# Kernel tuning notes

Measured on AMD Instinct MI355X. Metric: run time of the kernel, lower is better.

## Reference

```python
import jax, jax.numpy as jnp
import numpy as np

N_MODES = 256
N_LAYERS = 4


def _fourier_layer(inp, x, fw_l, lw_l):
    # inp: [B, n_modes] layer state; x: [B, 3] coords
    # tf.signal.rfftnd(..., fft_length=[n_modes]) crops/pads the last axis to
    # n_modes, i.e. uses the first n_modes entries of concat([x, inp], -1).
    d = jnp.concatenate([x, inp], axis=-1)[:, :N_MODES]        # [B, n_modes]
    F = jnp.fft.rfft(d, n=N_MODES, axis=-1)                    # [B, n_modes//2+1]
    x_spatial = jnp.fft.irfft(F * fw_l.astype(F.dtype), n=N_MODES, axis=-1)
    x_spatial = x_spatial.astype(jnp.float32)
    z = inp[:, :N_MODES] * lw_l                                # linear residual branch
    return jax.nn.relu(x_spatial + z)


def setup_inputs() -> dict:
    key = jax.random.key(0)
    ks = jax.random.split(key, 6)
    B, P1, P2, P3 = 262144, 64, N_MODES, 1
    mu = jax.random.normal(ks[0], (B, P1), dtype=jnp.float32)
    x = jax.random.normal(ks[1], (B, 3), dtype=jnp.float32)
    W1 = jax.random.normal(ks[2], (P1, P2), dtype=jnp.float32) * (2.0 / P1) ** 0.5
    b1 = jnp.zeros((P2,), dtype=jnp.float32)
    fw = jax.random.normal(ks[3], (N_LAYERS, N_MODES // 2 + 1), dtype=jnp.float32)
    lw = jax.random.normal(ks[4], (N_LAYERS, N_MODES), dtype=jnp.float32) * 0.1
    W2 = jax.random.normal(ks[5], (P2, P3), dtype=jnp.float32) * (1.0 / P2) ** 0.5
    b2 = jnp.zeros((P3,), dtype=jnp.float32)
    return {"mu": mu, "x": x, "W1": W1, "b1": b1, "fw": fw, "lw": lw, "W2": W2, "b2": b2}


def reference(mu, x, W1, b1, fw, lw, W2, b2):
    # encoder (first_network): dense + relu  -> [B, p_2]
    h = jax.nn.relu(mu @ W1 + b1)
    # stack of Fourier layers (small, structurally distinct loop over n_layers)
    for l in range(N_LAYERS):
        h = _fourier_layer(h, x, fw[l], lw[l])
    # decoder (last_network): dense -> [B, p_3]
    return h @ W2 + b2
```

## Files before the change

### kernel.cpp

```cpp
#include <hip/hip_runtime.h>

#define N_B   262144
#define BM    128
#define KAUG  288
#define LDA   264
#define LHX   32

typedef _Float16 f16x8 __attribute__((ext_vector_type(8)));
typedef _Float16 f16x4 __attribute__((ext_vector_type(4)));
typedef float    f32x4 __attribute__((ext_vector_type(4)));

__global__ void fno_precompute(const float* __restrict__ W1,
                               const float* __restrict__ fw,
                               const float* __restrict__ lw,
                               _Float16* __restrict__ Mt,
                               _Float16* __restrict__ W1t)
{
    const int t = threadIdx.x;
    const int b = blockIdx.x;
    if (b < 64) {
        const int l  = b >> 4;
        const int ng = b & 15;
        __shared__ float cosTab[256];
        __shared__ float cs[256];
        cosTab[t] = cosf((float)t * (6.28318530717958647692f / 256.0f));
        __syncthreads();
        {
            const float* fwl = fw + l * 129;
            float s = fwl[0];
            #pragma unroll 4
            for (int k = 1; k < 128; ++k)
                s += 2.0f * fwl[k] * cosTab[(k * t) & 255];
            s += fwl[128] * ((t & 1) ? -1.0f : 1.0f);
            cs[t] = s * (1.0f / 256.0f);
        }
        __syncthreads();
        for (int idx = t; idx < 16 * KAUG; idx += 256) {
            const int n = ng * 16 + idx / KAUG;
            const int k = idx % KAUG;
            float v = 0.0f;
            if (k < 253)               v = cs[(n - k - 3) & 255];
            if (k == n)                v += lw[l * 256 + n];
            if (k >= 256 && k < 259)   v = cs[(n - (k - 256)) & 255];
            Mt[((size_t)l * 256 + n) * KAUG + k] = (_Float16)v;
        }
    } else {
        const int base = (b - 64) * 4096;
        #pragma unroll
        for (int i = 0; i < 16; ++i) {
            const int idx = base + t + i * 256;
            const int n = idx >> 6, k = idx & 63;
            W1t[idx] = (_Float16)W1[k * 256 + n];
        }
    }
}

__global__ __launch_bounds__(256, 2)
void fno_main(const float* __restrict__ mu,
              const float* __restrict__ x,
              const float* __restrict__ b1,
              const float* __restrict__ W2,
              const float* __restrict__ b2,
              const _Float16* __restrict__ Mt,
              const _Float16* __restrict__ W1t,
              float* __restrict__ out)
{
    __shared__ __align__(16) _Float16 hA[BM * LDA];
    __shared__ __align__(16) _Float16 hxA[BM * LHX];
    __shared__ float b1s[256];
    __shared__ float W2s[256];
    __shared__ float red[BM];

    const int t    = threadIdx.x;
    const int w    = t >> 6;
    const int lane = t & 63;
    const int i16  = lane & 15;
    const int q    = lane >> 4;
    const int r0   = blockIdx.x * BM;

    {
        const float4* mu4 = (const float4*)mu + (size_t)r0 * 16;
        #pragma unroll
        for (int j = 0; j < 8; ++j) {
            int f = t + 256 * j;
            int row = f >> 4, c4 = f & 15;
            float4 v = mu4[f];
            f16x4 h;
            h[0] = (_Float16)v.x; h[1] = (_Float16)v.y;
            h[2] = (_Float16)v.z; h[3] = (_Float16)v.w;
            *(f16x4*)&hA[row * LDA + c4 * 4] = h;
        }
        f16x8 z8 = {(_Float16)0, (_Float16)0, (_Float16)0, (_Float16)0,
                    (_Float16)0, (_Float16)0, (_Float16)0, (_Float16)0};
        #pragma unroll
        for (int j = 0; j < 2; ++j)
            *(f16x8*)&hxA[(t + 256 * j) * 8] = z8;
    }
    __syncthreads();
    if (t < BM) {
        const float* xp = x + (size_t)(r0 + t) * 3;
        hxA[t * LHX + 0] = (_Float16)xp[0];
        hxA[t * LHX + 1] = (_Float16)xp[1];
        hxA[t * LHX + 2] = (_Float16)xp[2];
    }
    b1s[t] = b1[t];
    W2s[t] = W2[t];
    __syncthreads();

    const f32x4 fz = {0.f, 0.f, 0.f, 0.f};
    f32x4 acc[4][8];

    #pragma unroll
    for (int ft = 0; ft < 4; ++ft)
        #pragma unroll
        for (int rt = 0; rt < 8; ++rt) acc[ft][rt] = fz;

    #pragma unroll
    for (int ks = 0; ks < 2; ++ks) {
        const int kb = ks * 32;
        f16x8 mfrag[4];
        #pragma unroll
        for (int ft = 0; ft < 4; ++ft) {
            int n = 64 * w + 16 * ft + i16;
            mfrag[ft] = *(const f16x8*)(W1t + n * 64 + kb + 8 * q);
        }
        #pragma unroll
        for (int rt = 0; rt < 8; ++rt) {
            f16x8 hfrag = *(const f16x8*)&hA[(16 * rt + i16) * LDA + kb + 8 * q];
            #pragma unroll
            for (int ft = 0; ft < 4; ++ft)
                acc[ft][rt] = __builtin_amdgcn_mfma_f32_16x16x32_f16(
                    mfrag[ft], hfrag, acc[ft][rt], 0, 0, 0);
        }
    }
    __syncthreads();
    #pragma unroll
    for (int ft = 0; ft < 4; ++ft) {
        const int f = 64 * w + 16 * ft + 4 * q;
        const float4 bias = *(const float4*)&b1s[f];
        #pragma unroll
        for (int rt = 0; rt < 8; ++rt) {
            const int row = 16 * rt + i16;
            f32x4 v = acc[ft][rt];
            f16x4 hv;
            hv[0] = (_Float16)fmaxf(v[0] + bias.x, 0.f);
            hv[1] = (_Float16)fmaxf(v[1] + bias.y, 0.f);
            hv[2] = (_Float16)fmaxf(v[2] + bias.z, 0.f);
            hv[3] = (_Float16)fmaxf(v[3] + bias.w, 0.f);
            *(f16x4*)&hA[row * LDA + f] = hv;
        }
    }

    #pragma unroll 1
    for (int l = 0; l < 4; ++l) {
        __syncthreads();
        #pragma unroll
        for (int ft = 0; ft < 4; ++ft)
            #pragma unroll
            for (int rt = 0; rt < 8; ++rt) acc[ft][rt] = fz;

        const _Float16* Ml = Mt + (size_t)l * 256 * KAUG;
        #pragma unroll
        for (int ks = 0; ks < 9; ++ks) {
            const int kb = ks * 32;
            f16x8 mfrag[4];
            #pragma unroll
            for (int ft = 0; ft < 4; ++ft) {
                int n = 64 * w + 16 * ft + i16;
                mfrag[ft] = *(const f16x8*)(Ml + n * KAUG + kb + 8 * q);
            }
            #pragma unroll
            for (int rt = 0; rt < 8; ++rt) {
                f16x8 hfrag;
                if (ks < 8)
                    hfrag = *(const f16x8*)&hA[(16 * rt + i16) * LDA + kb + 8 * q];
                else
                    hfrag = *(const f16x8*)&hxA[(16 * rt + i16) * LHX + 8 * q];
                #pragma unroll
                for (int ft = 0; ft < 4; ++ft)
                    acc[ft][rt] = __builtin_amdgcn_mfma_f32_16x16x32_f16(
                        mfrag[ft], hfrag, acc[ft][rt], 0, 0, 0);
            }
        }
        __syncthreads();
        #pragma unroll
        for (int ft = 0; ft < 4; ++ft) {
            const int f = 64 * w + 16 * ft + 4 * q;
            #pragma unroll
            for (int rt = 0; rt < 8; ++rt) {
                const int row = 16 * rt + i16;
                f32x4 v = acc[ft][rt];
                f16x4 hv;
                hv[0] = (_Float16)fmaxf(v[0], 0.f);
                hv[1] = (_Float16)fmaxf(v[1], 0.f);
                hv[2] = (_Float16)fmaxf(v[2], 0.f);
                hv[3] = (_Float16)fmaxf(v[3], 0.f);
                *(f16x4*)&hA[row * LDA + f] = hv;
            }
        }
    }

    __syncthreads();
    {
        const int r  = t & 127;
        const int hf = t >> 7;
        const int n0 = hf * 128;
        float s = 0.f;
        #pragma unroll
        for (int j = 0; j < 16; ++j) {
            f16x8 v = *(const f16x8*)&hA[r * LDA + n0 + 8 * j];
            const float* wp = &W2s[n0 + 8 * j];
            s += (float)v[0] * wp[0] + (float)v[1] * wp[1]
               + (float)v[2] * wp[2] + (float)v[3] * wp[3]
               + (float)v[4] * wp[4] + (float)v[5] * wp[5]
               + (float)v[6] * wp[6] + (float)v[7] * wp[7];
        }
        if (hf) red[r] = s;
        __syncthreads();
        if (!hf) out[r0 + r] = s + red[r] + b2[0];
    }
}

extern "C" void kernel_launch(void* const* d_in, const int* in_sizes, int n_in,
                              void* d_out, int out_size, void* d_ws, size_t ws_size,
                              hipStream_t stream) {
    const float* mu = (const float*)d_in[0];
    const float* x  = (const float*)d_in[1];
    const float* W1 = (const float*)d_in[2];
    const float* b1 = (const float*)d_in[3];
    const float* fw = (const float*)d_in[4];
    const float* lw = (const float*)d_in[5];
    const float* W2 = (const float*)d_in[6];
    const float* b2 = (const float*)d_in[7];
    float* out = (float*)d_out;

    _Float16* Mt  = (_Float16*)d_ws;
    _Float16* W1t = Mt + 4 * 256 * KAUG;

    fno_precompute<<<68, 256, 0, stream>>>(W1, fw, lw, Mt, W1t);
    fno_main<<<N_B / BM, 256, 0, stream>>>(mu, x, b1, W2, b2, Mt, W1t, out);
}
```

Before: 237.5 us.

## Exploit circulant structure: build MFMA weight fragments from LDS shifted-cosine table

Instead of materializing a full 256x288 fp16 circulant-plus-diagonal matrix per layer in global memory, the precompute writes 8 shifted copies of the 256-entry circulant kernel, and the main kernel loads fragments for each layer from that small table held in LDS. The x coordinates are stored in columns 253-255 of the activation tile, with the displaced columns moved to a side slot at 260, so each layer needs 8 K-steps instead of 9. The diagonal linear branch moves to the epilogue as a per-element FMA with lw held in LDS. This removes global/L2 traffic for the weight matrix and one MFMA K-step per layer, at the cost of extra index arithmetic, an extra LDS read in the epilogue, and a per-layer reload of the table.

```diff
diff --git a/kernel.cpp b/kernel.cpp
--- a/kernel.cpp
+++ b/kernel.cpp
@@ -2,9 +2,7 @@
 
 #define N_B   262144
 #define BM    128
-#define KAUG  288
 #define LDA   264
-#define LHX   32
 
 typedef _Float16 f16x8 __attribute__((ext_vector_type(8)));
 typedef _Float16 f16x4 __attribute__((ext_vector_type(4)));
@@ -12,40 +10,30 @@
 
 __global__ void fno_precompute(const float* __restrict__ W1,
                                const float* __restrict__ fw,
-                               const float* __restrict__ lw,
-                               _Float16* __restrict__ Mt,
+                               _Float16* __restrict__ csr8G,
                                _Float16* __restrict__ W1t)
 {
     const int t = threadIdx.x;
     const int b = blockIdx.x;
-    if (b < 64) {
-        const int l  = b >> 4;
-        const int ng = b & 15;
+    if (b < 4) {
+        const int l = b;
         __shared__ float cosTab[256];
         __shared__ float cs[256];
         cosTab[t] = cosf((float)t * (6.28318530717958647692f / 256.0f));
         __syncthreads();
-        {
-            const float* fwl = fw + l * 129;
-            float s = fwl[0];
-            #pragma unroll 4
-            for (int k = 1; k < 128; ++k)
-                s += 2.0f * fwl[k] * cosTab[(k * t) & 255];
-            s += fwl[128] * ((t & 1) ? -1.0f : 1.0f);
-            cs[t] = s * (1.0f / 256.0f);
-        }
-        __syncthreads();
-        for (int idx = t; idx < 16 * KAUG; idx += 256) {
-            const int n = ng * 16 + idx / KAUG;
-            const int k = idx % KAUG;
-            float v = 0.0f;
-            if (k < 253)               v = cs[(n - k - 3) & 255];
-            if (k == n)                v += lw[l * 256 + n];
-            if (k >= 256 && k < 259)   v = cs[(n - (k - 256)) & 255];
-            Mt[((size_t)l * 256 + n) * KAUG + k] = (_Float16)v;
-        }
+        const float* fwl = fw + l * 129;
+        float s = fwl[0];
+        #pragma unroll 4
+        for (int k = 1; k < 128; ++k)
+            s += 2.0f * fwl[k] * cosTab[(k * t) & 255];
+        s += fwl[128] * ((t & 1) ? -1.0f : 1.0f);
+        cs[t] = s * (1.0f / 256.0f);
+        __syncthreads();
+        #pragma unroll
+        for (int p = 0; p < 8; ++p)
+            csr8G[(l * 8 + p) * 256 + t] = (_Float16)cs[(256 - (t + p)) & 255];
     } else {
-        const int base = (b - 64) * 4096;
+        const int base = (b - 4) * 4096;
         #pragma unroll
         for (int i = 0; i < 16; ++i) {
             const int idx = base + t + i * 256;
@@ -59,16 +47,18 @@
 void fno_main(const float* __restrict__ mu,
               const float* __restrict__ x,
               const float* __restrict__ b1,
+              const float* __restrict__ lw,
               const float* __restrict__ W2,
               const float* __restrict__ b2,
-              const _Float16* __restrict__ Mt,
+              const _Float16* __restrict__ csr8G,
               const _Float16* __restrict__ W1t,
               float* __restrict__ out)
 {
     __shared__ __align__(16) _Float16 hA[BM * LDA];
-    __shared__ __align__(16) _Float16 hxA[BM * LHX];
+    __shared__ __align__(16) _Float16 csr8[8 * 264];
+    __shared__ float lws[4 * 256];
     __shared__ float b1s[256];
-    __shared__ float W2s[256];
+    __shared__ float W2s[260];
     __shared__ float red[BM];
 
     const int t    = threadIdx.x;
@@ -77,6 +67,9 @@
     const int i16  = lane & 15;
     const int q    = lane >> 4;
     const int r0   = blockIdx.x * BM;
+    const int hoff = i16 * LDA + 8 * q;
+    const int p8   = t >> 5;
+    const int i08  = (t & 31) * 8;
 
     {
         const float4* mu4 = (const float4*)mu + (size_t)r0 * 16;
@@ -90,21 +83,21 @@
             h[2] = (_Float16)v.z; h[3] = (_Float16)v.w;
             *(f16x4*)&hA[row * LDA + c4 * 4] = h;
         }
-        f16x8 z8 = {(_Float16)0, (_Float16)0, (_Float16)0, (_Float16)0,
-                    (_Float16)0, (_Float16)0, (_Float16)0, (_Float16)0};
-        #pragma unroll
-        for (int j = 0; j < 2; ++j)
-            *(f16x8*)&hxA[(t + 256 * j) * 8] = z8;
-    }
-    __syncthreads();
-    if (t < BM) {
-        const float* xp = x + (size_t)(r0 + t) * 3;
-        hxA[t * LHX + 0] = (_Float16)xp[0];
-        hxA[t * LHX + 1] = (_Float16)xp[1];
-        hxA[t * LHX + 2] = (_Float16)xp[2];
-    }
-    b1s[t] = b1[t];
-    W2s[t] = W2[t];
+        if (t < BM) {
+            const float* xp = x + (size_t)(r0 + t) * 3;
+            hA[t * LDA + 253] = (_Float16)xp[0];
+            hA[t * LDA + 254] = (_Float16)xp[1];
+            hA[t * LDA + 255] = (_Float16)xp[2];
+        }
+        *(f16x8*)&csr8[p8 * 264 + i08] = *(const f16x8*)&csr8G[p8 * 256 + i08];
+        lws[t]       = lw[t];
+        lws[256 + t] = lw[256 + t];
+        lws[512 + t] = lw[512 + t];
+        lws[768 + t] = lw[768 + t];
+        b1s[t] = b1[t];
+        W2s[t] = (t < 253) ? W2[t] : 0.0f;
+        if (t < 4) W2s[256 + t] = W2[252 + t];
+    }
     __syncthreads();
 
     const f32x4 fz = {0.f, 0.f, 0.f, 0.f};
@@ -117,7 +110,7 @@
 
     #pragma unroll
     for (int ks = 0; ks < 2; ++ks) {
-        const int kb = ks * 32;
+        const int kb = 32 * ks;
         f16x8 mfrag[4];
         #pragma unroll
         for (int ft = 0; ft < 4; ++ft) {
@@ -126,7 +119,7 @@
         }
         #pragma unroll
         for (int rt = 0; rt < 8; ++rt) {
-            f16x8 hfrag = *(const f16x8*)&hA[(16 * rt + i16) * LDA + kb + 8 * q];
+            f16x8 hfrag = *(const f16x8*)&hA[hoff + 16 * rt * LDA + kb];
             #pragma unroll
             for (int ft = 0; ft < 4; ++ft)
                 acc[ft][rt] = __builtin_amdgcn_mfma_f32_16x16x32_f16(
@@ -147,9 +140,16 @@
             hv[1] = (_Float16)fmaxf(v[1] + bias.y, 0.f);
             hv[2] = (_Float16)fmaxf(v[2] + bias.z, 0.f);
             hv[3] = (_Float16)fmaxf(v[3] + bias.w, 0.f);
-            *(f16x4*)&hA[row * LDA + f] = hv;
-        }
-    }
+            if (f == 252) {
+                hA[row * LDA + 252] = hv[0];
+                *(f16x4*)&hA[row * LDA + 260] = hv;
+            } else {
+                *(f16x4*)&hA[row * LDA + f] = hv;
+            }
+        }
+    }
+
+    const int bl = (3 + 8 * q - 64 * w - i16) & 255;
 
     #pragma unroll 1
     for (int l = 0; l < 4; ++l) {
@@ -159,43 +159,52 @@
             #pragma unroll
             for (int rt = 0; rt < 8; ++rt) acc[ft][rt] = fz;
 
-        const _Float16* Ml = Mt + (size_t)l * 256 * KAUG;
-        #pragma unroll
-        for (int ks = 0; ks < 9; ++ks) {
-            const int kb = ks * 32;
-            f16x8 mfrag[4];
+        #pragma unroll
+        for (int ks = 0; ks < 8; ++ks) {
+            const int kb = 32 * ks;
+            f16x8 mf[4];
             #pragma unroll
             for (int ft = 0; ft < 4; ++ft) {
-                int n = 64 * w + 16 * ft + i16;
-                mfrag[ft] = *(const f16x8*)(Ml + n * KAUG + kb + 8 * q);
+                const int j0 = (bl + kb + 256 - 16 * ft) & 255;
+                mf[ft] = *(const f16x8*)&csr8[(j0 & 7) * 264 + (j0 & 248)];
             }
             #pragma unroll
             for (int rt = 0; rt < 8; ++rt) {
-                f16x8 hfrag;
-                if (ks < 8)
-                    hfrag = *(const f16x8*)&hA[(16 * rt + i16) * LDA + kb + 8 * q];
-                else
-                    hfrag = *(const f16x8*)&hxA[(16 * rt + i16) * LHX + 8 * q];
+                f16x8 hfrag = *(const f16x8*)&hA[hoff + 16 * rt * LDA + kb];
                 #pragma unroll
                 for (int ft = 0; ft < 4; ++ft)
                     acc[ft][rt] = __builtin_amdgcn_mfma_f32_16x16x32_f16(
-                        mfrag[ft], hfrag, acc[ft][rt], 0, 0, 0);
-            }
-        }
-        __syncthreads();
+                        mf[ft], hfrag, acc[ft][rt], 0, 0, 0);
+            }
+        }
+        __syncthreads();
+
+        if (l < 3)
+            *(f16x8*)&csr8[p8 * 264 + i08] =
+                *(const f16x8*)&csr8G[((l + 1) * 8 + p8) * 256 + i08];
+
+        const float* lwl = lws + l * 256;
         #pragma unroll
         for (int ft = 0; ft < 4; ++ft) {
             const int f = 64 * w + 16 * ft + 4 * q;
+            const float4 lw4 = *(const float4*)&lwl[f];
             #pragma unroll
             for (int rt = 0; rt < 8; ++rt) {
                 const int row = 16 * rt + i16;
+                const int za = row * LDA + ((f == 252) ? 260 : f);
+                f16x4 hp = *(const f16x4*)&hA[za];
                 f32x4 v = acc[ft][rt];
                 f16x4 hv;
-                hv[0] = (_Float16)fmaxf(v[0], 0.f);
-                hv[1] = (_Float16)fmaxf(v[1], 0.f);
-                hv[2] = (_Float16)fmaxf(v[2], 0.f);
-                hv[3] = (_Float16)fmaxf(v[3], 0.f);
-                *(f16x4*)&hA[row * LDA + f] = hv;
+                hv[0] = (_Float16)fmaxf(v[0] + lw4.x * (float)hp[0], 0.f);
+                hv[1] = (_Float16)fmaxf(v[1] + lw4.y * (float)hp[1], 0.f);
+                hv[2] = (_Float16)fmaxf(v[2] + lw4.z * (float)hp[2], 0.f);
+                hv[3] = (_Float16)fmaxf(v[3] + lw4.w * (float)hp[3], 0.f);
+                if (f == 252) {
+                    hA[row * LDA + 252] = hv[0];
+                    *(f16x4*)&hA[row * LDA + 260] = hv;
+                } else {
+                    *(f16x4*)&hA[row * LDA + f] = hv;
+                }
             }
         }
     }
@@ -215,7 +224,12 @@
                + (float)v[4] * wp[4] + (float)v[5] * wp[5]
                + (float)v[6] * wp[6] + (float)v[7] * wp[7];
         }
-        if (hf) red[r] = s;
+        if (hf) {
+            f16x4 st = *(const f16x4*)&hA[r * LDA + 260];
+            s += (float)st[1] * W2s[257] + (float)st[2] * W2s[258]
+               + (float)st[3] * W2s[259];
+            red[r] = s;
+        }
         __syncthreads();
         if (!hf) out[r0 + r] = s + red[r] + b2[0];
     }
@@ -234,9 +248,9 @@
     const float* b2 = (const float*)d_in[7];
     float* out = (float*)d_out;
 
-    _Float16* Mt  = (_Float16*)d_ws;
-    _Float16* W1t = Mt + 4 * 256 * KAUG;
-
-    fno_precompute<<<68, 256, 0, stream>>>(W1, fw, lw, Mt, W1t);
-    fno_main<<<N_B / BM, 256, 0, stream>>>(mu, x, b1, W2, b2, Mt, W1t, out);
+    _Float16* csr8G = (_Float16*)d_ws;
+    _Float16* W1t   = csr8G + 4 * 8 * 256;
+
+    fno_precompute<<<8, 256, 0, stream>>>(W1, fw, csr8G, W1t);
+    fno_main<<<N_B / BM, 256, 0, stream>>>(mu, x, b1, lw, W2, b2, csr8G, W1t, out);
 }
```

Measured after the change: 236.0 us. Within noise of the previous version (-0.6%).
